# Performance work log

Hardware: AMD Instinct MI355X
Metric: run time of the kernel (lower is better)

Reference implementation:

```python
import jax, jax.numpy as jnp
import numpy as np

L, B, N, D, H = 18, 2, 1024, 256, 4
DH = D // H  # head_dim = 64
LAYER_TYPES = ("self", "cross") * 9
BN_EPS = 1e-5


def setup_inputs() -> dict:
    key = jax.random.key(0)
    ks = jax.random.split(key, 8)
    s = 0.03  # small init scale keeps 18 residual layers numerically tame
    w = lambda k, shape: jax.random.normal(k, shape, jnp.float32) * s
    return dict(
        descriptors=jax.random.normal(ks[0], (B, 2, N, D), jnp.float32),
        mask=jnp.ones((B, 2, N), jnp.int32),
        qw=w(ks[1], (L, D, D)), qb=jnp.zeros((L, D), jnp.float32),
        kw=w(ks[2], (L, D, D)), kb=jnp.zeros((L, D), jnp.float32),
        vw=w(ks[3], (L, D, D)), vb=jnp.zeros((L, D), jnp.float32),
        ow=w(ks[4], (L, D, D)), ob=jnp.zeros((L, D), jnp.float32),
        w1=w(ks[5], (L, 2 * D, 2 * D)), b1=jnp.zeros((L, 2 * D), jnp.float32),
        bn_g=jnp.ones((L, 2 * D), jnp.float32), bn_b=jnp.zeros((L, 2 * D), jnp.float32),
        w2=w(ks[6], (L, 2 * D, D)), b2=jnp.zeros((L, D), jnp.float32),
    )


def _attention(x, src, m, i, qw, qb, kw, kb, vw, vb, ow, ob):
    b, n, d = x.shape
    q = (x @ qw[i] + qb[i]).reshape(b, n, H, DH)
    k = (src @ kw[i] + kb[i]).reshape(b, -1, H, DH)
    v = (src @ vw[i] + vb[i]).reshape(b, -1, H, DH)
    scores = jnp.einsum("bnhd,bmhd->bhnm", q, k) / (DH ** 0.5)
    scores = jnp.where(m[:, None, None, :] == 0, jnp.float32(-1e9), scores)
    probs = jax.nn.softmax(scores, axis=-1)  # fp32, matches torch dtype=float32
    out = jnp.einsum("bhnm,bmhd->bnhd", probs, v).reshape(b, n, d)
    return out @ ow[i] + ob[i]


def _propagate(x, src, m, i, qw, qb, kw, kb, vw, vb, ow, ob, w1, b1, bn_g, bn_b, w2, b2):
    a = _attention(x, src, m, i, qw, qb, kw, kb, vw, vb, ow, ob)
    h = jnp.concatenate([x, a], axis=-1)        # [B, N, 2D]
    h = h @ w1[i] + b1[i]                       # [B, N, 2D]
    # BatchNorm1d (training mode): per-channel stats over batch and keypoint dims
    mean = h.mean(axis=(0, 1))
    var = ((h - mean) ** 2).mean(axis=(0, 1))   # biased variance, as torch BN uses
    h = (h - mean) / jnp.sqrt(var + BN_EPS) * bn_g[i] + bn_b[i]
    h = jax.nn.relu(h)
    return h @ w2[i] + b2[i]                    # [B, N, D]


def reference(descriptors, mask, qw, qb, kw, kb, vw, vb, ow, ob, w1, b1, bn_g, bn_b, w2, b2):
    d0, d1 = descriptors[:, 0], descriptors[:, 1]
    m0, m1 = mask[:, 0], mask[:, 1]
    params = (qw, qb, kw, kb, vw, vb, ow, ob, w1, b1, bn_g, bn_b, w2, b2)
    for i, lt in enumerate(LAYER_TYPES):
        if lt == "cross":
            s0, s1, sm0, sm1 = d1, d0, m1, m0
        else:  # self
            s0, s1, sm0, sm1 = d0, d1, m0, m1
        delta0 = _propagate(d0, s0, sm0, i, *params)
        delta1 = _propagate(d1, s1, sm1, i, *params)
        d0 = d0 + delta0
        d1 = d1 + delta1
    return jnp.stack([d0, d1], axis=1)
```

## Files before the change

kernel.cpp:

```cpp
#include <hip/hip_runtime.h>


typedef __attribute__((ext_vector_type(8))) short bf16x8;
typedef __attribute__((ext_vector_type(4))) short bf16x4;
typedef __attribute__((ext_vector_type(4))) float floatx4;

__device__ __forceinline__ short f2b(float f) {
  unsigned u = __builtin_bit_cast(unsigned, f);
  unsigned r = (u + 0x7FFFu + ((u >> 16) & 1u)) >> 16;
  return (short)r;
}
__device__ __forceinline__ unsigned pack2(float a, float b) {
  return (unsigned)(unsigned short)f2b(a) | ((unsigned)(unsigned short)f2b(b) << 16);
}
__device__ __forceinline__ void split2(float a, float b, unsigned& h, unsigned& l) {
  unsigned short ha = (unsigned short)f2b(a), hb = (unsigned short)f2b(b);
  float fa = __builtin_bit_cast(float, (unsigned)ha << 16);
  float fb = __builtin_bit_cast(float, (unsigned)hb << 16);
  h = (unsigned)ha | ((unsigned)hb << 16);
  l = pack2(a - fa, b - fb);
}

__device__ __forceinline__ void gl2lds16(const void* g, void* l) {
  __builtin_amdgcn_global_load_lds(
      (const __attribute__((address_space(1))) unsigned*)g,
      (__attribute__((address_space(3))) unsigned*)l, 16, 0, 0);
}

__device__ __forceinline__ floatx4 mfma16_bf16(bf16x4 a, bf16x4 b, floatx4 c) {
#if __has_builtin(__builtin_amdgcn_mfma_f32_16x16x16_bf16)
  return __builtin_amdgcn_mfma_f32_16x16x16_bf16(a, b, c, 0, 0, 0);
#elif __has_builtin(__builtin_amdgcn_mfma_f32_16x16x16bf16_1k)
  return __builtin_amdgcn_mfma_f32_16x16x16bf16_1k(a, b, c, 0, 0, 0);
#else
  asm volatile("v_mfma_f32_16x16x16_bf16 %0, %1, %2, %0" : "+v"(c) : "v"(a), "v"(b));
  return c;
#endif
}

#define BARW   asm volatile("s_barrier" ::: "memory")
#define WAITV8 asm volatile("s_waitcnt vmcnt(8)" ::: "memory")
#define WAITV0 asm volatile("s_waitcnt vmcnt(0)" ::: "memory")
#define LGKM0  asm volatile("s_waitcnt lgkmcnt(0)" ::: "memory")
#define PRIO1  __builtin_amdgcn_s_setprio(1)
#define PRIO0  __builtin_amdgcn_s_setprio(0)

#define GEMM_IDS                                        \
  const int tid = threadIdx.x;                          \
  const int lane = tid & 63, w = tid >> 6;              \
  const int wy = w >> 1, wx = w & 1;                    \
  const int quad = lane >> 4, l16 = lane & 15;          \
  const int lr = lane >> 3;                             \
  const int lcs = (((lane & 7) ^ lr) & 7) * 8;          \
  const floatx4 z4 = {0.f, 0.f, 0.f, 0.f};

__device__ __forceinline__ void mfma_step_sw(const short* As, const short* Bs,
                                             int wy, int wx, int quad, int l16,
                                             floatx4 acc[2][4]) {
#pragma unroll
  for (int kk = 0; kk < 2; ++kk) {
    const int sw = (((kk * 4 + quad) ^ (l16 & 7)) * 8);
    bf16x8 a0 = *(const bf16x8*)&As[(wy * 32 + l16) * 64 + sw];
    bf16x8 a1 = *(const bf16x8*)&As[(wy * 32 + 16 + l16) * 64 + sw];
    bf16x8 b[4];
#pragma unroll
    for (int ni = 0; ni < 4; ++ni)
      b[ni] = *(const bf16x8*)&Bs[(wx * 64 + ni * 16 + l16) * 64 + sw];
#pragma unroll
    for (int ni = 0; ni < 4; ++ni) {
      acc[0][ni] = __builtin_amdgcn_mfma_f32_16x16x32_bf16(a0, b[ni], acc[0][ni], 0, 0, 0);
      acc[1][ni] = __builtin_amdgcn_mfma_f32_16x16x32_bf16(a1, b[ni], acc[1][ni], 0, 0, 0);
    }
  }
}

__device__ __forceinline__ void mfma_step_sw32(const short* As, const short* Bs,
                                               int wy, int wx, int quad, int l16,
                                               floatx4 acc[4]) {
#pragma unroll
  for (int kk = 0; kk < 2; ++kk) {
    const int sw = (((kk * 4 + quad) ^ (l16 & 7)) * 8);
    bf16x8 a0 = *(const bf16x8*)&As[(wy * 16 + l16) * 64 + sw];
    bf16x8 b[4];
#pragma unroll
    for (int ni = 0; ni < 4; ++ni)
      b[ni] = *(const bf16x8*)&Bs[(wx * 64 + ni * 16 + l16) * 64 + sw];
#pragma unroll
    for (int ni = 0; ni < 4; ++ni)
      acc[ni] = __builtin_amdgcn_mfma_f32_16x16x32_bf16(a0, b[ni], acc[ni], 0, 0, 0);
  }
}

__device__ __forceinline__ void mfma_step_sw32x64(const short* As, const short* Bs,
                                                  int wy, int wx, int quad, int l16,
                                                  floatx4 acc[2]) {
#pragma unroll
  for (int kk = 0; kk < 2; ++kk) {
    const int sw = (((kk * 4 + quad) ^ (l16 & 7)) * 8);
    bf16x8 a0 = *(const bf16x8*)&As[(wy * 16 + l16) * 64 + sw];
    bf16x8 b[2];
#pragma unroll
    for (int ni = 0; ni < 2; ++ni)
      b[ni] = *(const bf16x8*)&Bs[(wx * 32 + ni * 16 + l16) * 64 + sw];
#pragma unroll
    for (int ni = 0; ni < 2; ++ni)
      acc[ni] = __builtin_amdgcn_mfma_f32_16x16x32_bf16(a0, b[ni], acc[ni], 0, 0, 0);
  }
}

__global__ __launch_bounds__(256) void wfuse(
    const float* __restrict__ ow, const float* __restrict__ w1,
    short* __restrict__ wbuf) {
  __shared__ short As_h[64 * 64], As_l[64 * 64];
  __shared__ short Bs_h[128 * 64], Bs_l[128 * 64];
  const int blk = blockIdx.x;
  const int layer = blk >> 4, sub = blk & 15;
  const int kp0 = (sub & 3) * 64, n0 = (sub >> 2) * 128;
  const float* A = ow + (size_t)layer * 65536;
  const float* Bw = w1 + (size_t)layer * 262144 + 256 * 512;
  short* w1t = wbuf + (size_t)layer * 655360 + 262144;
  GEMM_IDS;
  (void)lr; (void)lcs;
  floatx4 acc[2][4] = {{z4, z4, z4, z4}, {z4, z4, z4, z4}};
  const int ar = tid >> 2, aq = tid & 3;
  const int bn = tid & 127, bkh = tid >> 7;

  for (int s = 0; s < 4; ++s) {
    const int k0 = s * 64;
    const float* Ar = &A[(size_t)(kp0 + ar) * 256 + k0 + aq * 16];
    float4 f0 = *(const float4*)&Ar[0];
    float4 f1 = *(const float4*)&Ar[4];
    float4 f2 = *(const float4*)&Ar[8];
    float4 f3 = *(const float4*)&Ar[12];
    float bv[32];
#pragma unroll
    for (int kk2 = 0; kk2 < 32; ++kk2)
      bv[kk2] = Bw[(size_t)(k0 + bkh * 32 + kk2) * 512 + n0 + bn];

    __syncthreads();
    {
      uint4 hi, lo;
      split2(f0.x, f0.y, hi.x, lo.x);
      split2(f0.z, f0.w, hi.y, lo.y);
      split2(f1.x, f1.y, hi.z, lo.z);
      split2(f1.z, f1.w, hi.w, lo.w);
      int sl = ((aq * 2) ^ (ar & 7)) * 8;
      *(uint4*)&As_h[ar * 64 + sl] = hi;
      *(uint4*)&As_l[ar * 64 + sl] = lo;
      split2(f2.x, f2.y, hi.x, lo.x);
      split2(f2.z, f2.w, hi.y, lo.y);
      split2(f3.x, f3.y, hi.z, lo.z);
      split2(f3.z, f3.w, hi.w, lo.w);
      sl = ((aq * 2 + 1) ^ (ar & 7)) * 8;
      *(uint4*)&As_h[ar * 64 + sl] = hi;
      *(uint4*)&As_l[ar * 64 + sl] = lo;
    }
#pragma unroll
    for (int cc = 0; cc < 4; ++cc) {
      uint4 hi, lo;
      split2(bv[cc * 8 + 0], bv[cc * 8 + 1], hi.x, lo.x);
      split2(bv[cc * 8 + 2], bv[cc * 8 + 3], hi.y, lo.y);
      split2(bv[cc * 8 + 4], bv[cc * 8 + 5], hi.z, lo.z);
      split2(bv[cc * 8 + 6], bv[cc * 8 + 7], hi.w, lo.w);
      int sl = ((bkh * 4 + cc) ^ (bn & 7)) * 8;
      *(uint4*)&Bs_h[bn * 64 + sl] = hi;
      *(uint4*)&Bs_l[bn * 64 + sl] = lo;
    }
    __syncthreads();
    mfma_step_sw(As_h, Bs_h, wy, wx, quad, l16, acc);
    mfma_step_sw(As_h, Bs_l, wy, wx, quad, l16, acc);
    mfma_step_sw(As_l, Bs_h, wy, wx, quad, l16, acc);
  }
#pragma unroll
  for (int mi = 0; mi < 2; ++mi)
#pragma unroll
    for (int ni = 0; ni < 4; ++ni) {
      int col = n0 + wx * 64 + ni * 16 + l16;
      int row0 = kp0 + wy * 32 + mi * 16 + quad * 4;
      uint2 uu;
      uu.x = pack2(acc[mi][ni][0], acc[mi][ni][1]);
      uu.y = pack2(acc[mi][ni][2], acc[mi][ni][3]);
      *(uint2*)&w1t[(size_t)col * 512 + 256 + row0] = uu;
    }
}

__global__ __launch_bounds__(256) void wprep(
    const float* __restrict__ qw, const float* __restrict__ kw,
    const float* __restrict__ vw, const float* __restrict__ w1,
    const float* __restrict__ w2, const float* __restrict__ ob,
    const float* __restrict__ b1, short* __restrict__ wbuf,
    float* __restrict__ beff, const float* __restrict__ desc,
    float* __restrict__ xd, short* __restrict__ xb,
    float* __restrict__ psz) {
  __shared__ float SH[64 * 130];
  int blk = blockIdx.x;
  int t = threadIdx.x;
  if (blk < 1296) {
    int layer = blk / 72;
    int sub = blk % 72;
    const float* W; int Kd, Nd, k0, n0; size_t ooff;
    if (sub < 24) {
      int wsel = sub / 8; int tt = sub & 7;
      k0 = (tt >> 1) * 64; n0 = (tt & 1) * 128; Kd = 256; Nd = 256;
      W = (wsel == 0 ? qw : wsel == 1 ? kw : vw) + (size_t)layer * 65536;
      ooff = (size_t)wsel * 65536;
    } else if (sub < 56) {
      int tt = sub - 24; k0 = (tt >> 2) * 64; n0 = (tt & 3) * 128;
      Kd = 512; Nd = 512; W = w1 + (size_t)layer * 262144; ooff = 262144;
    } else {
      int tt = sub - 56; k0 = (tt >> 1) * 64; n0 = (tt & 1) * 128;
      Kd = 512; Nd = 256; W = w2 + (size_t)layer * 131072; ooff = 524288;
    }
    short* out = wbuf + (size_t)layer * 655360 + ooff;
    const int rr = t >> 4;
    const int c4 = (t & 15) * 4;
#pragma unroll
    for (int i = 0; i < 4; ++i)
#pragma unroll
      for (int hf = 0; hf < 2; ++hf) {
        float4 v = *(const float4*)&W[(size_t)(k0 + i * 16 + rr) * Nd + n0 + hf * 64 + c4];
        float* tp = &SH[(i * 16 + rr) * 130 + hf * 64 + c4];
        tp[0] = v.x; tp[1] = v.y; tp[2] = v.z; tp[3] = v.w;
      }
    __syncthreads();
    const int n = t >> 1;
    const int kh = (t & 1) * 32;
    float v[32];
#pragma unroll
    for (int kk = 0; kk < 32; ++kk)
      v[kk] = SH[(kh + kk) * 130 + n];
    unsigned u[16];
#pragma unroll
    for (int j2 = 0; j2 < 16; ++j2) u[j2] = pack2(v[2 * j2], v[2 * j2 + 1]);
    short* op = &out[(size_t)(n0 + n) * Kd + k0 + kh];
#pragma unroll
    for (int q4 = 0; q4 < 4; ++q4) {
      uint4 o; o.x = u[q4 * 4]; o.y = u[q4 * 4 + 1]; o.z = u[q4 * 4 + 2]; o.w = u[q4 * 4 + 3];
      *(uint4*)&op[q4 * 8] = o;
    }
  } else if (blk < 1440) {
    int bb = blk - 1296;
    int layer = bb >> 3;
    int n0 = (bb & 7) * 64;
    const float* obL = ob + (size_t)layer * 256;
    const float* w1L = w1 + (size_t)layer * 262144 + 256 * 512;
    int n = n0 + (t & 63);
    int part = t >> 6;
    float s = 0.f;
    for (int i = part * 64; i < part * 64 + 64; ++i)
      s += obL[i] * w1L[(size_t)i * 512 + n];
    SH[part * 64 + (t & 63)] = s;
    __syncthreads();
    if (t < 64) {
      float tot = SH[t] + SH[64 + t] + SH[128 + t] + SH[192 + t] +
                  b1[(size_t)layer * 512 + n0 + t];
      beff[(size_t)layer * 512 + n0 + t] = tot;
    }
  } else if (blk < 2464) {
    int idx = (blk - 1440) * 256 + t;
    int fi = idx << 2;
    int hi = (fi >> 19) & 1;
    int lo = (fi >> 18) & 1;
    int sj = (fi & ~(3 << 18)) | (lo << 19) | (hi << 18);
    float4 v = *(const float4*)&desc[sj];
    *(float4*)&xd[fi] = v;
    uint2 uu; uu.x = pack2(v.x, v.y); uu.y = pack2(v.z, v.w);
    *(uint2*)&xb[fi] = uu;
  } else {
    int idx = (blk - 2464) * 1024 + t * 4;
    float4 zz = {0.f, 0.f, 0.f, 0.f};
    *(float4*)&psz[idx] = zz;
  }
}

__global__ __launch_bounds__(256, 2) void gemm_qkv(
    const short* __restrict__ xb, const short* __restrict__ wbufL,
    const float* __restrict__ qb_, const float* __restrict__ kb_,
    const float* __restrict__ vb_,
    short* __restrict__ q, short* __restrict__ kout, short* __restrict__ vT,
    int cross) {
  __shared__ short SM[40960];
  short* As = SM;
  short* Bs = SM + 8192;
  const int rb = blockIdx.x * 32;
  const int cb = blockIdx.y * 128;
  const int seg = cb >> 8;
  const int cbl = cb & 255;
  int arb = rb;
  if (seg) arb = (rb & 2047) | ((((rb >> 11) ^ cross) & 1) << 11);
  const short* A = xb + (size_t)arb * 256;
  const short* Wt = wbufL + (size_t)seg * 65536 + (size_t)cbl * 256;
  const float* bias = (seg == 0 ? qb_ : seg == 1 ? kb_ : vb_) + cbl;
  GEMM_IDS;
  floatx4 acc[4] = {z4, z4, z4, z4};

#pragma unroll
  for (int s = 0; s < 4; ++s) {
    const int k0 = s * 64;
    gl2lds16(&A[(size_t)(w * 8 + lr) * 256 + k0 + lcs], &As[s * 2048 + (w * 8) * 64]);
#pragma unroll
    for (int i = 0; i < 4; ++i)
      gl2lds16(&Wt[(size_t)(i * 32 + w * 8 + lr) * 256 + k0 + lcs],
               &Bs[s * 8192 + (i * 32 + w * 8) * 64]);
  }
  WAITV0;
  BARW;
#pragma unroll
  for (int s = 0; s < 4; ++s)
    mfma_step_sw32(&As[s * 2048], &Bs[s * 8192], wy, wx, quad, l16, acc);

  if (seg < 2) {
    short* C = (seg == 0 ? q : kout) + (size_t)rb * 256 + cbl;
#pragma unroll
    for (int ni = 0; ni < 4; ++ni) {
      int col = wx * 64 + ni * 16 + l16;
      float bc = bias[col];
#pragma unroll
      for (int reg = 0; reg < 4; ++reg) {
        int row = wy * 16 + quad * 4 + reg;
        C[(size_t)row * 256 + col] = f2b(acc[ni][reg] + bc);
      }
    }
  } else {
    BARW;
    short* T = SM + w * 1536;
    const int sb = rb >> 10;
    const int hh = (cbl >> 6) + wx;
    const int z = sb * 4 + hh;
#pragma unroll
    for (int ni = 0; ni < 4; ++ni) {
      int col = wx * 64 + ni * 16 + l16;
      float bc = bias[col];
#pragma unroll
      for (int reg = 0; reg < 4; ++reg)
        T[(ni * 16 + l16) * 24 + quad * 4 + reg] = f2b(acc[ni][reg] + bc);
    }
    short* dst = &vT[((size_t)z * 64 + lane) * 1024 + (rb & 1023) + wy * 16];
    *(uint4*)&dst[0] = *(const uint4*)&T[lane * 24 + 0];
    *(uint4*)&dst[8] = *(const uint4*)&T[lane * 24 + 8];
  }
}

__global__ __launch_bounds__(256) void attn_mfma(
    const short* __restrict__ q, const short* __restrict__ k,
    const short* __restrict__ vT, const int* __restrict__ mask,
    short* __restrict__ attnb, int cross) {
  __shared__ short Ks[2][2][4096];
  __shared__ short Vs[2][2][4096];
  __shared__ float Msk[1024];
  const int tid = threadIdx.x;
  const int lane = tid & 63, w = tid >> 6;
  const int wv = w & 1, wq = w >> 1;
  const int quad = lane >> 4, l16 = lane & 15;
  const int lr = lane >> 3;
  const int lcs = (((lane & 7) ^ lr) & 7) * 8;
  const int qt = blockIdx.x;
  const int z = blockIdx.y;
  const int sb = z >> 2, h = z & 3;
  const int s = sb >> 1, b = sb & 1;
  const int rowbase = sb * 1024;
  const int* mp = mask + (b * 2 + (s ^ cross)) * 1024;

  const int qrow = qt * 32 + wq * 16 + l16;
  bf16x8 qf[2];
#pragma unroll
  for (int kk = 0; kk < 2; ++kk)
    qf[kk] = *(const bf16x8*)&q[(size_t)(rowbase + qrow) * 256 + h * 64 + kk * 32 + quad * 8];

  {
    int4 mv = *(const int4*)&mp[tid * 4];
    Msk[tid * 4 + 0] = (mv.x == 0) ? -1.0e9f : 0.f;
    Msk[tid * 4 + 1] = (mv.y == 0) ? -1.0e9f : 0.f;
    Msk[tid * 4 + 2] = (mv.z == 0) ? -1.0e9f : 0.f;
    Msk[tid * 4 + 3] = (mv.w == 0) ? -1.0e9f : 0.f;
  }

  const floatx4 z4 = {0.f, 0.f, 0.f, 0.f};
  floatx4 o4[4] = {z4, z4, z4, z4};
  float mrun = -1e30f, lsum = 0.f;

#define ATT_STAGE(t, buf)                                                               \
  {                                                                                     \
    int key0s = wv * 512 + (t) * 64;                                                    \
    _Pragma("unroll") for (int j = 0; j < 4; ++j) {                                     \
      gl2lds16(&k[(size_t)(rowbase + key0s + j * 16 + wq * 8 + lr) * 256 + h * 64 + lcs], \
               &Ks[buf][wv][(j * 16 + wq * 8) * 64]);                                   \
      gl2lds16(&vT[((size_t)z * 64 + j * 16 + wq * 8 + lr) * 1024 + key0s + lcs],       \
               &Vs[buf][wv][(j * 16 + wq * 8) * 64]);                                   \
    }                                                                                   \
  }

  ATT_STAGE(0, 0);
  __syncthreads();
  for (int t = 0; t < 8; ++t) {
    int buf = t & 1;
    if (t < 7) { ATT_STAGE(t + 1, buf ^ 1); WAITV8; } else { WAITV0; }
    BARW;
    const int key0 = wv * 512 + t * 64;

    floatx4 sA[4] = {z4, z4, z4, z4};
    PRIO1;
#pragma unroll
    for (int kk = 0; kk < 2; ++kk) {
      const int sw = (((kk * 4 + quad) ^ (l16 & 7)) * 8);
#pragma unroll
      for (int mt = 0; mt < 4; ++mt) {
        bf16x8 kf = *(const bf16x8*)&Ks[buf][wv][(mt * 16 + l16) * 64 + sw];
        sA[mt] = __builtin_amdgcn_mfma_f32_16x16x32_bf16(kf, qf[kk], sA[mt], 0, 0, 0);
      }
    }
    PRIO0;
    float scv[4][4];
    float tmax = -1e30f;
#pragma unroll
    for (int mt = 0; mt < 4; ++mt) {
      float4 mk = *(const float4*)&Msk[key0 + mt * 16 + quad * 4];
      scv[mt][0] = sA[mt][0] * 0.125f + mk.x;
      scv[mt][1] = sA[mt][1] * 0.125f + mk.y;
      scv[mt][2] = sA[mt][2] * 0.125f + mk.z;
      scv[mt][3] = sA[mt][3] * 0.125f + mk.w;
#pragma unroll
      for (int reg = 0; reg < 4; ++reg) tmax = fmaxf(tmax, scv[mt][reg]);
    }
    tmax = fmaxf(tmax, __shfl_xor(tmax, 16));
    tmax = fmaxf(tmax, __shfl_xor(tmax, 32));
    float mnew = fmaxf(mrun, tmax);
    float corr = __expf(mrun - mnew);
    mrun = mnew;
    lsum *= corr;
#pragma unroll
    for (int dt = 0; dt < 4; ++dt)
#pragma unroll
      for (int reg = 0; reg < 4; ++reg) o4[dt][reg] *= corr;

    bf16x4 pb[4];
#pragma unroll
    for (int mt = 0; mt < 4; ++mt) {
      float e0 = __expf(scv[mt][0] - mnew);
      float e1 = __expf(scv[mt][1] - mnew);
      float e2 = __expf(scv[mt][2] - mnew);
      float e3 = __expf(scv[mt][3] - mnew);
      lsum += (e0 + e1) + (e2 + e3);
      union { bf16x4 v; uint2 u; } pu;
      pu.u.x = pack2(e0, e1); pu.u.y = pack2(e2, e3);
      pb[mt] = pu.v;
    }
    PRIO1;
#pragma unroll
    for (int mt = 0; mt < 4; ++mt) {
      const int c2 = mt * 2 + (quad >> 1);
      const int sub = (quad & 1) * 4;
#pragma unroll
      for (int dt = 0; dt < 4; ++dt) {
        bf16x4 vf = *(const bf16x4*)&Vs[buf][wv][(dt * 16 + l16) * 64 +
                                                 ((c2 ^ (l16 & 7)) * 8) + sub];
        o4[dt] = mfma16_bf16(vf, pb[mt], o4[dt]);
      }
    }
    PRIO0;
    LGKM0;
    BARW;
  }
  lsum += __shfl_xor(lsum, 16);
  lsum += __shfl_xor(lsum, 32);

  float* MG = (float*)&Ks[0][0][0];
  const int mo = (wq * 64 + lane) * 18;
  if (wv == 1) {
    MG[mo] = mrun;
    MG[mo + 1] = lsum;
#pragma unroll
    for (int dt = 0; dt < 4; ++dt)
#pragma unroll
      for (int reg = 0; reg < 4; ++reg) MG[mo + 2 + dt * 4 + reg] = o4[dt][reg];
  }
  __syncthreads();
  if (wv == 0) {
    float m2 = MG[mo], l2 = MG[mo + 1];
    float mm = fmaxf(mrun, m2);
    float ca = __expf(mrun - mm), cb2 = __expf(m2 - mm);
    float inv = 1.f / (ca * lsum + cb2 * l2);
    short* op = &attnb[(size_t)(rowbase + qrow) * 256 + h * 64 + quad * 4];
#pragma unroll
    for (int dt = 0; dt < 4; ++dt) {
      float v0 = (ca * o4[dt][0] + cb2 * MG[mo + 2 + dt * 4 + 0]) * inv;
      float v1 = (ca * o4[dt][1] + cb2 * MG[mo + 2 + dt * 4 + 1]) * inv;
      float v2 = (ca * o4[dt][2] + cb2 * MG[mo + 2 + dt * 4 + 2]) * inv;
      float v3 = (ca * o4[dt][3] + cb2 * MG[mo + 2 + dt * 4 + 3]) * inv;
      uint2 uu;
      uu.x = pack2(v0, v1);
      uu.y = pack2(v2, v3);
      *(uint2*)&op[dt * 16] = uu;
    }
  }
#undef ATT_STAGE
}

__global__ __launch_bounds__(256, 2) void gemm_w1(
    const short* __restrict__ xb, const short* __restrict__ attnb,
    const short* __restrict__ w1t, const float* __restrict__ beff,
    float* __restrict__ hbuf, float* __restrict__ psumL, float* __restrict__ psqL) {
  __shared__ short SM[40960];
  short* As = SM;
  short* Bs = SM + 8192;
  const int rb = blockIdx.x * 32, cb = blockIdx.y * 128;
  const int str = rb >> 11;
  GEMM_IDS;
  floatx4 acc[4] = {z4, z4, z4, z4};

#pragma unroll
  for (int h = 0; h < 2; ++h) {
    if (h) BARW;
    const short* Ap = (h == 0 ? xb : attnb) + (size_t)rb * 256;
#pragma unroll
    for (int st = 0; st < 4; ++st) {
      const int k0 = h * 256 + st * 64;
      gl2lds16(&Ap[(size_t)(w * 8 + lr) * 256 + st * 64 + lcs],
               &As[st * 2048 + (w * 8) * 64]);
#pragma unroll
      for (int i = 0; i < 4; ++i)
        gl2lds16(&w1t[(size_t)(cb + i * 32 + w * 8 + lr) * 512 + k0 + lcs],
                 &Bs[st * 8192 + (i * 32 + w * 8) * 64]);
    }
    WAITV0;
    BARW;
#pragma unroll
    for (int st = 0; st < 4; ++st)
      mfma_step_sw32(&As[st * 2048], &Bs[st * 8192], wy, wx, quad, l16, acc);
  }

  float colsum[4], colsq[4];
#pragma unroll
  for (int ni = 0; ni < 4; ++ni) { colsum[ni] = 0.f; colsq[ni] = 0.f; }
#pragma unroll
  for (int ni = 0; ni < 4; ++ni) {
    int col = wx * 64 + ni * 16 + l16;
    float bc = beff[cb + col];
#pragma unroll
    for (int reg = 0; reg < 4; ++reg) {
      int row = rb + wy * 16 + quad * 4 + reg;
      float val = acc[ni][reg] + bc;
      hbuf[(size_t)row * 512 + cb + col] = val;
      colsum[ni] += val; colsq[ni] += val * val;
    }
  }
#pragma unroll
  for (int ni = 0; ni < 4; ++ni)
#pragma unroll
    for (int d = 16; d < 64; d <<= 1) {
      colsum[ni] += __shfl_xor(colsum[ni], d);
      colsq[ni]  += __shfl_xor(colsq[ni], d);
    }
  __syncthreads();
  float (*Ps)[2][128] = (float(*)[2][128])SM;
  if (quad == 0) {
#pragma unroll
    for (int ni = 0; ni < 4; ++ni) {
      Ps[wy][0][wx * 64 + ni * 16 + l16] = colsum[ni];
      Ps[wy][1][wx * 64 + ni * 16 + l16] = colsq[ni];
    }
  }
  __syncthreads();
  if (tid < 128) {
    atomicAdd(&psumL[str * 512 + cb + tid], Ps[0][0][tid] + Ps[1][0][tid]);
    atomicAdd(&psqL [str * 512 + cb + tid], Ps[0][1][tid] + Ps[1][1][tid]);
  }
}

__global__ __launch_bounds__(256, 3) void gemm_w2(
    const float* __restrict__ hbuf, const short* __restrict__ w2t,
    const float* __restrict__ b2_, const float* __restrict__ psumL,
    const float* __restrict__ psqL, const float* __restrict__ g,
    const float* __restrict__ be, float* __restrict__ xd, short* __restrict__ xb,
    float* __restrict__ outp) {
  __shared__ short SM[24576];
  __shared__ float s_scale[512], s_shift[512];
  short* As = SM;
  short* Bs = SM + 8192;
  const int rb = blockIdx.x * 32, cb = blockIdx.y * 64;
  const int str = rb >> 11;
  GEMM_IDS;
  floatx4 acc[2] = {z4, z4};
#pragma unroll
  for (int cc = 0; cc < 2; ++cc) {
    int c = tid + cc * 256;
    float sum = psumL[str * 512 + c];
    float sq  = psqL [str * 512 + c];
    float mean = sum * (1.f / 2048.f);
    float var = sq * (1.f / 2048.f) - mean * mean;
    float rstd = rsqrtf(var + 1e-5f);
    float gs = g[c] * rstd;
    s_scale[c] = gs;
    s_shift[c] = be[c] - mean * gs;
  }
  __syncthreads();

  const int p = tid & 7, ar = tid >> 3;

#pragma unroll
  for (int h = 0; h < 2; ++h) {
    if (h) BARW;
#pragma unroll
    for (int st = 0; st < 4; ++st) {
      const int k0 = h * 256 + st * 64;
#pragma unroll
      for (int i = 0; i < 2; ++i)
        gl2lds16(&w2t[(size_t)(cb + i * 32 + w * 8 + lr) * 512 + k0 + lcs],
                 &Bs[st * 4096 + (i * 32 + w * 8) * 64]);
    }
#pragma unroll
    for (int st = 0; st < 4; ++st) {
      const int cs = h * 256 + st * 64 + ((p ^ (ar & 7)) * 8);
      float4 h0 = *(const float4*)&hbuf[(size_t)(rb + ar) * 512 + cs];
      float4 h1 = *(const float4*)&hbuf[(size_t)(rb + ar) * 512 + cs + 4];
      float4 sc0 = *(const float4*)&s_scale[cs];
      float4 sc1 = *(const float4*)&s_scale[cs + 4];
      float4 sh0 = *(const float4*)&s_shift[cs];
      float4 sh1 = *(const float4*)&s_shift[cs + 4];
      uint4 pk;
      pk.x = pack2(fmaxf(h0.x * sc0.x + sh0.x, 0.f), fmaxf(h0.y * sc0.y + sh0.y, 0.f));
      pk.y = pack2(fmaxf(h0.z * sc0.z + sh0.z, 0.f), fmaxf(h0.w * sc0.w + sh0.w, 0.f));
      pk.z = pack2(fmaxf(h1.x * sc1.x + sh1.x, 0.f), fmaxf(h1.y * sc1.y + sh1.y, 0.f));
      pk.w = pack2(fmaxf(h1.z * sc1.z + sh1.z, 0.f), fmaxf(h1.w * sc1.w + sh1.w, 0.f));
      *(uint4*)&As[st * 2048 + ar * 64 + p * 8] = pk;
    }
    WAITV0;
    LGKM0;
    BARW;
#pragma unroll
    for (int st = 0; st < 4; ++st)
      mfma_step_sw32x64(&As[st * 2048], &Bs[st * 4096], wy, wx, quad, l16, acc);
  }

#pragma unroll
  for (int ni = 0; ni < 2; ++ni) {
    int col = cb + wx * 32 + ni * 16 + l16;
    float bc = b2_[col];
#pragma unroll
    for (int reg = 0; reg < 4; ++reg) {
      int row = rb + wy * 16 + quad * 4 + reg;
      float r = xd[(size_t)row * 256 + col] + acc[ni][reg] + bc;
      xd[(size_t)row * 256 + col] = r;
      xb[(size_t)row * 256 + col] = f2b(r);
      if (outp) {
        int ss = row >> 11, bb = (row >> 10) & 1, n = row & 1023;
        outp[(size_t)((bb * 2 + ss) * 1024 + n) * 256 + col] = r;
      }
    }
  }
}

extern "C" void kernel_launch(void* const* d_in, const int* in_sizes, int n_in,
                              void* d_out, int out_size, void* d_ws, size_t ws_size,
                              hipStream_t stream) {
  (void)in_sizes; (void)n_in; (void)out_size; (void)ws_size;
  const float* desc = (const float*)d_in[0];
  const int*   mask = (const int*)d_in[1];
  const float* qw = (const float*)d_in[2];
  const float* qb = (const float*)d_in[3];
  const float* kw = (const float*)d_in[4];
  const float* kb = (const float*)d_in[5];
  const float* vw = (const float*)d_in[6];
  const float* vb = (const float*)d_in[7];
  const float* ow = (const float*)d_in[8];
  const float* ob = (const float*)d_in[9];
  const float* w1 = (const float*)d_in[10];
  const float* b1 = (const float*)d_in[11];
  const float* bn_g = (const float*)d_in[12];
  const float* bn_b = (const float*)d_in[13];
  const float* w2 = (const float*)d_in[14];
  const float* b2 = (const float*)d_in[15];
  float* out = (float*)d_out;

  char* base = (char*)d_ws;
  float* xd    = (float*)(base);
  float* hbuf  = (float*)(base + (4u << 20));
  short* xb    = (short*)(base + (12u << 20));
  short* qb16  = (short*)(base + (14u << 20));
  short* kb16  = (short*)(base + (16u << 20));
  short* vTb   = (short*)(base + (18u << 20));
  short* attnb = (short*)(base + (20u << 20));
  float* psum  = (float*)(base + (22u << 20));
  float* psq   = psum + 18 * 1024;
  float* beff  = psq + 18 * 1024;
  short* wbuf  = (short*)(base + (24u << 20));

  wprep<<<2500, 256, 0, stream>>>(qw, kw, vw, w1, w2, ob, b1,
                                  wbuf, beff, desc, xd, xb, psum);
  wfuse<<<288, 256, 0, stream>>>(ow, w1, wbuf);

  for (int i = 0; i < 18; ++i) {
    int cross = i & 1;
    short* wb = wbuf + (size_t)i * 655360;

    gemm_qkv<<<dim3(128, 6), 256, 0, stream>>>(
        xb, wb, qb + (size_t)i * 256, kb + (size_t)i * 256, vb + (size_t)i * 256,
        qb16, kb16, vTb, cross);
    attn_mfma<<<dim3(32, 16), 256, 0, stream>>>(qb16, kb16, vTb, mask, attnb, cross);
    gemm_w1<<<dim3(128, 4), 256, 0, stream>>>(xb, attnb, wb + 262144,
                                              beff + (size_t)i * 512,
                                              hbuf, psum + (size_t)i * 1024,
                                              psq + (size_t)i * 1024);
    gemm_w2<<<dim3(128, 4), 256, 0, stream>>>(hbuf, wb + 524288,
                                              b2 + (size_t)i * 256,
                                              psum + (size_t)i * 1024,
                                              psq + (size_t)i * 1024,
                                              bn_g + (size_t)i * 512,
                                              bn_b + (size_t)i * 512, xd, xb,
                                              (i == 17) ? out : nullptr);
  }
}
```

Before: 933.0 us.

## Single-buffer V tiles in attention for higher occupancy; split weight-prep blocks

The attention kernel now keeps only one V tile buffer per wave-half and loads the next V tile after the PV MMAs instead of alongside K. This cuts LDS use so that three blocks per CU can be resident, which the launch bounds now request. The cost is an extra wait and barrier per iteration and less prefetch distance for V. Separately, the weight-prep kernel is split into half-K blocks with a smaller shared tile to get more, lighter blocks.

```diff
diff --git a/kernel.cpp b/kernel.cpp
--- a/kernel.cpp
+++ b/kernel.cpp
@@ -40,6 +40,7 @@
 
 #define BARW   asm volatile("s_barrier" ::: "memory")
 #define WAITV8 asm volatile("s_waitcnt vmcnt(8)" ::: "memory")
+#define WAITV4 asm volatile("s_waitcnt vmcnt(4)" ::: "memory")
 #define WAITV0 asm volatile("s_waitcnt vmcnt(0)" ::: "memory")
 #define LGKM0  asm volatile("s_waitcnt lgkmcnt(0)" ::: "memory")
 #define PRIO1  __builtin_amdgcn_s_setprio(1)
@@ -192,12 +193,14 @@
     float* __restrict__ beff, const float* __restrict__ desc,
     float* __restrict__ xd, short* __restrict__ xb,
     float* __restrict__ psz) {
-  __shared__ float SH[64 * 130];
+  __shared__ float SH[32 * 130];
   int blk = blockIdx.x;
   int t = threadIdx.x;
-  if (blk < 1296) {
-    int layer = blk / 72;
-    int sub = blk % 72;
+  if (blk < 2592) {
+    int layer = blk / 144;
+    int sub2 = blk % 144;
+    int sub = sub2 >> 1;
+    int khalf = sub2 & 1;
     const float* W; int Kd, Nd, k0, n0; size_t ooff;
     if (sub < 24) {
       int wsel = sub / 8; int tt = sub & 7;
@@ -211,11 +214,12 @@
       int tt = sub - 56; k0 = (tt >> 1) * 64; n0 = (tt & 1) * 128;
       Kd = 512; Nd = 256; W = w2 + (size_t)layer * 131072; ooff = 524288;
     }
+    k0 += khalf * 32;
     short* out = wbuf + (size_t)layer * 655360 + ooff;
     const int rr = t >> 4;
     const int c4 = (t & 15) * 4;
 #pragma unroll
-    for (int i = 0; i < 4; ++i)
+    for (int i = 0; i < 2; ++i)
 #pragma unroll
       for (int hf = 0; hf < 2; ++hf) {
         float4 v = *(const float4*)&W[(size_t)(k0 + i * 16 + rr) * Nd + n0 + hf * 64 + c4];
@@ -224,22 +228,21 @@
       }
     __syncthreads();
     const int n = t >> 1;
-    const int kh = (t & 1) * 32;
-    float v[32];
-#pragma unroll
-    for (int kk = 0; kk < 32; ++kk)
+    const int kh = (t & 1) * 16;
+    float v[16];
+#pragma unroll
+    for (int kk = 0; kk < 16; ++kk)
       v[kk] = SH[(kh + kk) * 130 + n];
-    unsigned u[16];
-#pragma unroll
-    for (int j2 = 0; j2 < 16; ++j2) u[j2] = pack2(v[2 * j2], v[2 * j2 + 1]);
+    unsigned u[8];
+#pragma unroll
+    for (int j2 = 0; j2 < 8; ++j2) u[j2] = pack2(v[2 * j2], v[2 * j2 + 1]);
     short* op = &out[(size_t)(n0 + n) * Kd + k0 + kh];
-#pragma unroll
-    for (int q4 = 0; q4 < 4; ++q4) {
-      uint4 o; o.x = u[q4 * 4]; o.y = u[q4 * 4 + 1]; o.z = u[q4 * 4 + 2]; o.w = u[q4 * 4 + 3];
-      *(uint4*)&op[q4 * 8] = o;
-    }
-  } else if (blk < 1440) {
-    int bb = blk - 1296;
+    uint4 o1; o1.x = u[0]; o1.y = u[1]; o1.z = u[2]; o1.w = u[3];
+    uint4 o2; o2.x = u[4]; o2.y = u[5]; o2.z = u[6]; o2.w = u[7];
+    *(uint4*)&op[0] = o1;
+    *(uint4*)&op[8] = o2;
+  } else if (blk < 2736) {
+    int bb = blk - 2592;
     int layer = bb >> 3;
     int n0 = (bb & 7) * 64;
     const float* obL = ob + (size_t)layer * 256;
@@ -256,8 +259,8 @@
                   b1[(size_t)layer * 512 + n0 + t];
       beff[(size_t)layer * 512 + n0 + t] = tot;
     }
-  } else if (blk < 2464) {
-    int idx = (blk - 1440) * 256 + t;
+  } else if (blk < 3760) {
+    int idx = (blk - 2736) * 256 + t;
     int fi = idx << 2;
     int hi = (fi >> 19) & 1;
     int lo = (fi >> 18) & 1;
@@ -267,7 +270,7 @@
     uint2 uu; uu.x = pack2(v.x, v.y); uu.y = pack2(v.z, v.w);
     *(uint2*)&xb[fi] = uu;
   } else {
-    int idx = (blk - 2464) * 1024 + t * 4;
+    int idx = (blk - 3760) * 1024 + t * 4;
     float4 zz = {0.f, 0.f, 0.f, 0.f};
     *(float4*)&psz[idx] = zz;
   }
@@ -341,12 +344,12 @@
   }
 }
 
-__global__ __launch_bounds__(256) void attn_mfma(
+__global__ __launch_bounds__(256, 3) void attn_mfma(
     const short* __restrict__ q, const short* __restrict__ k,
     const short* __restrict__ vT, const int* __restrict__ mask,
     short* __restrict__ attnb, int cross) {
   __shared__ short Ks[2][2][4096];
-  __shared__ short Vs[2][2][4096];
+  __shared__ short Vs[2][4096];
   __shared__ float Msk[1024];
   const int tid = threadIdx.x;
   const int lane = tid & 63, w = tid >> 6;
@@ -379,22 +382,27 @@
   floatx4 o4[4] = {z4, z4, z4, z4};
   float mrun = -1e30f, lsum = 0.f;
 
-#define ATT_STAGE(t, buf)                                                               \
+#define ATT_STAGE_K(t, buf)                                                             \
   {                                                                                     \
     int key0s = wv * 512 + (t) * 64;                                                    \
-    _Pragma("unroll") for (int j = 0; j < 4; ++j) {                                     \
+    _Pragma("unroll") for (int j = 0; j < 4; ++j)                                       \
       gl2lds16(&k[(size_t)(rowbase + key0s + j * 16 + wq * 8 + lr) * 256 + h * 64 + lcs], \
                &Ks[buf][wv][(j * 16 + wq * 8) * 64]);                                   \
+  }
+#define ATT_STAGE_V(t)                                                                  \
+  {                                                                                     \
+    int key0s = wv * 512 + (t) * 64;                                                    \
+    _Pragma("unroll") for (int j = 0; j < 4; ++j)                                       \
       gl2lds16(&vT[((size_t)z * 64 + j * 16 + wq * 8 + lr) * 1024 + key0s + lcs],       \
-               &Vs[buf][wv][(j * 16 + wq * 8) * 64]);                                   \
-    }                                                                                   \
-  }
-
-  ATT_STAGE(0, 0);
+               &Vs[wv][(j * 16 + wq * 8) * 64]);                                        \
+  }
+
+  ATT_STAGE_K(0, 0);
+  ATT_STAGE_V(0);
   __syncthreads();
   for (int t = 0; t < 8; ++t) {
     int buf = t & 1;
-    if (t < 7) { ATT_STAGE(t + 1, buf ^ 1); WAITV8; } else { WAITV0; }
+    if (t < 7) { ATT_STAGE_K(t + 1, buf ^ 1); WAITV8; } else { WAITV4; }
     BARW;
     const int key0 = wv * 512 + t * 64;
 
@@ -445,6 +453,8 @@
       pu.u.x = pack2(e0, e1); pu.u.y = pack2(e2, e3);
       pb[mt] = pu.v;
     }
+    if (t < 7) { WAITV4; } else { WAITV0; }
+    BARW;
     PRIO1;
 #pragma unroll
     for (int mt = 0; mt < 4; ++mt) {
@@ -452,14 +462,15 @@
       const int sub = (quad & 1) * 4;
 #pragma unroll
       for (int dt = 0; dt < 4; ++dt) {
-        bf16x4 vf = *(const bf16x4*)&Vs[buf][wv][(dt * 16 + l16) * 64 +
-                                                 ((c2 ^ (l16 & 7)) * 8) + sub];
+        bf16x4 vf = *(const bf16x4*)&Vs[wv][(dt * 16 + l16) * 64 +
+                                            ((c2 ^ (l16 & 7)) * 8) + sub];
         o4[dt] = mfma16_bf16(vf, pb[mt], o4[dt]);
       }
     }
     PRIO0;
     LGKM0;
     BARW;
+    if (t < 7) ATT_STAGE_V(t + 1);
   }
   lsum += __shfl_xor(lsum, 16);
   lsum += __shfl_xor(lsum, 32);
@@ -493,7 +504,8 @@
       *(uint2*)&op[dt * 16] = uu;
     }
   }
-#undef ATT_STAGE
+#undef ATT_STAGE_K
+#undef ATT_STAGE_V
 }
 
 __global__ __launch_bounds__(256, 2) void gemm_w1(
@@ -685,7 +697,7 @@
   float* beff  = psq + 18 * 1024;
   short* wbuf  = (short*)(base + (24u << 20));
 
-  wprep<<<2500, 256, 0, stream>>>(qw, kw, vw, w1, w2, ob, b1,
+  wprep<<<3796, 256, 0, stream>>>(qw, kw, vw, w1, w2, ob, b1,
                                   wbuf, beff, desc, xd, xb, psum);
   wfuse<<<288, 256, 0, stream>>>(ow, w1, wbuf);
 
```

Result: no change. 923.2 us (-1.0%).
